# Kernel optimization log

Measured on AMD Instinct MI355X. Metric: run time of the kernel, lower is better.

The kernel has to match this reference:

```python
import jax, jax.numpy as jnp
import numpy as np

N = 50000      # num nodes
E = 400000     # num directed edges
IN = 128       # in_channels
H = 256        # hidden_channels
OUT = 128      # out_channels
LN_EPS = 1e-5


def setup_inputs() -> dict:
    key = jax.random.key(0)
    ks = jax.random.split(key, 12)
    x = jax.random.normal(ks[0], (N, IN), jnp.float32)
    edge_index = jax.random.randint(ks[1], (2, E), 0, N, jnp.int32)

    def lin(k, fi, fo):
        return jax.random.normal(k, (fi, fo), jnp.float32) / jnp.sqrt(jnp.float32(fi))

    return {
        "x": x,
        "edge_index": edge_index,
        "W1": lin(ks[2], IN, H),  "b1": jnp.zeros((H,), jnp.float32),
        "W2": lin(ks[3], H, H),   "b2": jnp.zeros((H,), jnp.float32),
        "W3": lin(ks[4], H, H),   "b3": jnp.zeros((H,), jnp.float32),
        "W4": lin(ks[5], H, OUT), "b4": jnp.zeros((OUT,), jnp.float32),
        "g1": jnp.ones((H,), jnp.float32),   "be1": jnp.zeros((H,), jnp.float32),
        "g2": jnp.ones((H,), jnp.float32),   "be2": jnp.zeros((H,), jnp.float32),
        "g3": jnp.ones((H,), jnp.float32),   "be3": jnp.zeros((H,), jnp.float32),
        "g4": jnp.ones((OUT,), jnp.float32), "be4": jnp.zeros((OUT,), jnp.float32),
    }


def layer_norm(h, g, b):
    m = jnp.mean(h, axis=-1, keepdims=True)
    v = jnp.mean(jnp.square(h - m), axis=-1, keepdims=True)
    return (h - m) * jax.lax.rsqrt(v + LN_EPS) * g + b


def gcn_conv(h, W, b, src, dst, dinv):
    # PyG GCNConv: add self-loops, norm = deg^-1/2[src] * deg^-1/2[dst]
    h = h @ W                                             # [N, F_out]
    norm = (dinv[src] * dinv[dst])[:, None]               # [E, 1]
    msg = h[src] * norm                                   # [E, F_out] irregular gather
    agg = jax.ops.segment_sum(msg, dst, num_segments=N)   # scatter-add
    agg = agg + h * jnp.square(dinv)[:, None]             # self-loop term
    return agg + b


def reference(x, edge_index, W1, b1, W2, b2, W3, b3, W4, b4,
              g1, be1, g2, be2, g3, be3, g4, be4):
    src, dst = edge_index[0], edge_index[1]
    # degree (incl. self-loop) from destination index, as in PyG gcn_norm
    deg = jax.ops.segment_sum(jnp.ones((E,), jnp.float32), dst, num_segments=N) + 1.0
    dinv = jax.lax.rsqrt(deg)

    h = gcn_conv(x, W1, b1, src, dst, dinv)
    h = jax.nn.relu(layer_norm(h, g1, be1))   # dropout = identity (eval)
    h = gcn_conv(h, W2, b2, src, dst, dinv)
    h = jax.nn.relu(layer_norm(h, g2, be2))
    h = gcn_conv(h, W3, b3, src, dst, dinv)
    h = jax.nn.relu(layer_norm(h, g3, be3))
    h = gcn_conv(h, W4, b4, src, dst, dinv)
    h = layer_norm(h, g4, be4)
    return h
```

## Files before the change

kernel.cpp:

```cpp
#include <hip/hip_runtime.h>

#define NN 50000
#define NEDGE 400000
#define MPAD 50048
#define NB 196
constexpr float LN_EPS = 1e-5f;

typedef __attribute__((ext_vector_type(8))) short bf16x8;
typedef __attribute__((ext_vector_type(4))) float f32x4;
typedef __attribute__((ext_vector_type(8))) unsigned short ushort8v;

__device__ __forceinline__ unsigned short f2bf(float f) {
  unsigned int u = __float_as_uint(f);
  u += 0x7FFFu + ((u >> 16) & 1u);
  return (unsigned short)(u >> 16);
}
__device__ __forceinline__ float bf2f(unsigned short u) {
  return __uint_as_float(((unsigned int)u) << 16);
}

__global__ __launch_bounds__(256) void k_prep(
    const float* __restrict__ W1, const float* __restrict__ W2,
    const float* __restrict__ W3, const float* __restrict__ W4,
    unsigned short* __restrict__ Wt1, unsigned short* __restrict__ Wt2,
    unsigned short* __restrict__ Wt3, unsigned short* __restrict__ Wt4,
    const float* __restrict__ x, unsigned short* __restrict__ xB,
    int* __restrict__ cnt) {
  const int b = blockIdx.x;
  const int n = threadIdx.x;
  if (b < 128) {
    Wt1[(size_t)n * 128 + b] = f2bf(W1[(size_t)b * 256 + n]);
  } else if (b < 384) {
    const int k = b - 128;
    Wt2[(size_t)n * 256 + k] = f2bf(W2[(size_t)k * 256 + n]);
  } else if (b < 640) {
    const int k = b - 384;
    Wt3[(size_t)n * 256 + k] = f2bf(W3[(size_t)k * 256 + n]);
  } else if (b < 896) {
    const int k = b - 640;
    if (n < 128) Wt4[(size_t)n * 256 + k] = f2bf(W4[(size_t)k * 128 + n]);
  } else if (b < 7146) {
    const int i = (b - 896) * 256 + n;
    float4 v = reinterpret_cast<const float4*>(x)[i];
    ushort4 o; o.x = f2bf(v.x); o.y = f2bf(v.y); o.z = f2bf(v.z); o.w = f2bf(v.w);
    reinterpret_cast<ushort4*>(xB)[i] = o;
  } else {
    const int i = (b - 7146) * 256 + n;
    if (i < NN) cnt[i] = 0;
  }
}

__global__ void k_count(const int* __restrict__ dst, int* __restrict__ cnt) {
  int e = blockIdx.x * blockDim.x + threadIdx.x;
  if (e < NEDGE) atomicAdd(&cnt[dst[e]], 1);
}

__global__ __launch_bounds__(256) void k_bsum(const int* __restrict__ cnt,
                                              int* __restrict__ bsum,
                                              float* __restrict__ dinv) {
  const int i = blockIdx.x * 256 + threadIdx.x;
  int v = 0;
  if (i < NN) {
    v = cnt[i];
    dinv[i] = rsqrtf((float)v + 1.0f);
  }
  int s = v;
#pragma unroll
  for (int off = 32; off > 0; off >>= 1) s += __shfl_xor(s, off);
  __shared__ int wsum[4];
  if ((threadIdx.x & 63) == 0) wsum[threadIdx.x >> 6] = s;
  __syncthreads();
  if (threadIdx.x == 0) bsum[blockIdx.x] = wsum[0] + wsum[1] + wsum[2] + wsum[3];
}

__global__ __launch_bounds__(256) void k_bapply(const int* __restrict__ cnt,
                                                const int* __restrict__ bsum,
                                                int* __restrict__ rowptr,
                                                int* __restrict__ cursor) {
  __shared__ int sOff[NB];
  __shared__ int wsum[4], woff[4];
  const int t = threadIdx.x;
  const int lane = t & 63, wid = t >> 6;

  {
    int v = (t < NB) ? bsum[t] : 0;
    int inc = v;
    for (int off = 1; off < 64; off <<= 1) {
      int y = __shfl_up(inc, off);
      if (lane >= off) inc += y;
    }
    if (lane == 63) wsum[wid] = inc;
    __syncthreads();
    if (t == 0) {
      int run = 0;
      for (int w = 0; w < 4; ++w) { woff[w] = run; run += wsum[w]; }
    }
    __syncthreads();
    if (t < NB) sOff[t] = woff[wid] + inc - v;
  }
  __syncthreads();

  const int i = blockIdx.x * 256 + t;
  int v = (i < NN) ? cnt[i] : 0;
  int inc = v;
  for (int off = 1; off < 64; off <<= 1) {
    int y = __shfl_up(inc, off);
    if (lane >= off) inc += y;
  }
  if (lane == 63) wsum[wid] = inc;
  __syncthreads();
  if (t == 0) {
    int run = 0;
    for (int w = 0; w < 4; ++w) { woff[w] = run; run += wsum[w]; }
  }
  __syncthreads();
  if (i < NN) {
    const int rp = sOff[blockIdx.x] + woff[wid] + inc - v;
    rowptr[i] = rp;
    cursor[i] = rp;
  }
  if (blockIdx.x == 0 && t == 0) rowptr[NN] = NEDGE;
}

__global__ void k_fill(const int* __restrict__ src, const int* __restrict__ dst,
                       const float* __restrict__ dinv, int* __restrict__ cursor,
                       int2* __restrict__ eidx2) {
  int e = blockIdx.x * blockDim.x + threadIdx.x;
  if (e >= NEDGE) return;
  const int d = dst[e];
  const int s = src[e];
  const int p = atomicAdd(&cursor[d], 1);
  eidx2[p] = make_int2(s, __float_as_int(dinv[s] * dinv[d]));
}

template<int F, int NPW, int MODE>
__global__ __launch_bounds__(256) void k_gather(
    const int* __restrict__ rowptr, const int2* __restrict__ eidx2,
    const float* __restrict__ dinv, const unsigned short* __restrict__ h,
    void* __restrict__ outv, const float* __restrict__ bias,
    const float* __restrict__ gamma, const float* __restrict__ beta) {
  constexpr int LPN = 64 / NPW;
  static_assert(F / LPN == 8, "16B per lane");
  const int tid = threadIdx.x;
  const int lane = tid & 63;
  const int sub = lane / LPN;
  const int slane = lane % LPN;
  const int n = blockIdx.x * (4 * NPW) + (tid >> 6) * NPW + sub;
  const bool valid = n < NN;

  int e = 0, end = 0;
  float dn = 0.f;
  if (valid) {
    dn = dinv[n];
    e = rowptr[n];
    end = rowptr[n + 1];
  }

  float acc[8];
  ushort8v r[8];
#pragma unroll
  for (int u = 0; u < 8; ++u) r[u] = (ushort8v)0;
  {
    ushort8v r0 = (ushort8v)0;
    if (valid) r0 = *reinterpret_cast<const ushort8v*>(h + (size_t)n * F + slane * 8);
    const float sw = dn * dn;
#pragma unroll
    for (int j = 0; j < 8; ++j) acc[j] = bf2f(r0[j]) * sw;
  }

  while (__ballot(e < end)) {
    float wgt[8];
#pragma unroll
    for (int u = 0; u < 8; ++u) {
      wgt[u] = 0.f;
      if (e + u < end) {
        const int2 p = eidx2[e + u];
        wgt[u] = __int_as_float(p.y);
        r[u] = *reinterpret_cast<const ushort8v*>(h + (size_t)p.x * F + slane * 8);
      }
    }
#pragma unroll
    for (int u = 0; u < 8; ++u)
#pragma unroll
      for (int j = 0; j < 8; ++j)
        acc[j] += wgt[u] * bf2f(r[u][j]);
    e += 8;
  }

  if (!valid) return;

  if constexpr (MODE == 0) {
    ushort8v o;
#pragma unroll
    for (int j = 0; j < 8; ++j) o[j] = f2bf(acc[j]);
    *reinterpret_cast<ushort8v*>((unsigned short*)outv + (size_t)n * F + slane * 8) = o;
  } else {
    const float4 b0 = *reinterpret_cast<const float4*>(bias + slane * 8);
    const float4 b1 = *reinterpret_cast<const float4*>(bias + slane * 8 + 4);
    acc[0] += b0.x; acc[1] += b0.y; acc[2] += b0.z; acc[3] += b0.w;
    acc[4] += b1.x; acc[5] += b1.y; acc[6] += b1.z; acc[7] += b1.w;
    float s = 0.f, q = 0.f;
#pragma unroll
    for (int j = 0; j < 8; ++j) { s += acc[j]; q = fmaf(acc[j], acc[j], q); }
#pragma unroll
    for (int off = 1; off < 16; off <<= 1) {
      s += __shfl_xor(s, off);
      q += __shfl_xor(q, off);
    }
    const float mean = s * (1.0f / 128.0f);
    const float var = q * (1.0f / 128.0f) - mean * mean;
    const float inv = rsqrtf(var + LN_EPS);
    const float4 g0 = *reinterpret_cast<const float4*>(gamma + slane * 8);
    const float4 g1 = *reinterpret_cast<const float4*>(gamma + slane * 8 + 4);
    const float4 e0 = *reinterpret_cast<const float4*>(beta + slane * 8);
    const float4 e1 = *reinterpret_cast<const float4*>(beta + slane * 8 + 4);
    float4 o0, o1;
    o0.x = (acc[0] - mean) * inv * g0.x + e0.x;
    o0.y = (acc[1] - mean) * inv * g0.y + e0.y;
    o0.z = (acc[2] - mean) * inv * g0.z + e0.z;
    o0.w = (acc[3] - mean) * inv * g0.w + e0.w;
    o1.x = (acc[4] - mean) * inv * g1.x + e1.x;
    o1.y = (acc[5] - mean) * inv * g1.y + e1.y;
    o1.z = (acc[6] - mean) * inv * g1.z + e1.z;
    o1.w = (acc[7] - mean) * inv * g1.w + e1.w;
    float* out = (float*)outv + (size_t)n * 128 + slane * 8;
    *reinterpret_cast<float4*>(out) = o0;
    *reinterpret_cast<float4*>(out + 4) = o1;
  }
}

template<int K, int N, bool LNFUSE>
__global__ __launch_bounds__(256) void k_mgemm(const unsigned short* __restrict__ A,
                                               const unsigned short* __restrict__ Bt,
                                               const float* __restrict__ bias,
                                               const float* __restrict__ gamma,
                                               const float* __restrict__ beta,
                                               unsigned short* __restrict__ out) {
  constexpr int NT = N / 64;
  constexpr int KS = K / 32;
  __shared__ __align__(16) unsigned short As[64 * K];

  const int tid = threadIdx.x;
  const int lane = tid & 63;
  const int w = tid >> 6;
  const int m0 = blockIdx.x * 64;

#pragma unroll
  for (int i = 0; i < KS; ++i) {
    const int o = (i * 256 + tid) * 16;
    const int row = o / (2 * K);
    const int inb = o % (2 * K);
    uint4 val = *reinterpret_cast<const uint4*>(
        (const char*)A + (size_t)(m0 + row) * (2 * K) + inb);
    const int dsto = o ^ ((row & 7) << 4);
    *reinterpret_cast<uint4*>((char*)As + dsto) = val;
  }
  __syncthreads();

  f32x4 acc[4][NT];
#pragma unroll
  for (int mt = 0; mt < 4; ++mt)
#pragma unroll
    for (int nt = 0; nt < NT; ++nt) acc[mt][nt] = (f32x4){0.f, 0.f, 0.f, 0.f};

  const int nw0 = w * (N / 4);
  const int arow = lane & 15;
  const int kgrp = (lane >> 4) * 8;

  for (int ks = 0; ks < KS; ++ks) {
    bf16x8 af[4];
#pragma unroll
    for (int mt = 0; mt < 4; ++mt) {
      const int r = mt * 16 + arow;
      int boff = (r * K + ks * 32 + kgrp) * 2;
      boff ^= (r & 7) << 4;
      af[mt] = *reinterpret_cast<const bf16x8*>((const char*)As + boff);
    }
    bf16x8 bfr[NT];
#pragma unroll
    for (int nt = 0; nt < NT; ++nt) {
      const int n = nw0 + nt * 16 + arow;
      bfr[nt] = *reinterpret_cast<const bf16x8*>(Bt + (size_t)n * K + ks * 32 + kgrp);
    }
#pragma unroll
    for (int mt = 0; mt < 4; ++mt)
#pragma unroll
      for (int nt = 0; nt < NT; ++nt)
        acc[mt][nt] = __builtin_amdgcn_mfma_f32_16x16x32_bf16(af[mt], bfr[nt], acc[mt][nt], 0, 0, 0);
  }

  const int g = lane >> 4;
  const int cl = lane & 15;

  if constexpr (LNFUSE) {
    float gv[NT], bev[NT];
#pragma unroll
    for (int nt = 0; nt < NT; ++nt) {
      const int c = nw0 + nt * 16 + cl;
      const float bv = bias[c];
      gv[nt] = gamma[c];
      bev[nt] = beta[c];
#pragma unroll
      for (int mt = 0; mt < 4; ++mt)
#pragma unroll
        for (int reg = 0; reg < 4; ++reg) acc[mt][nt][reg] += bv;
    }
    __shared__ float sS[4][64];
    __shared__ float sQ[4][64];
    float ps[4][4], pq[4][4];
#pragma unroll
    for (int mt = 0; mt < 4; ++mt) {
#pragma unroll
      for (int reg = 0; reg < 4; ++reg) {
        float s = 0.f, q = 0.f;
#pragma unroll
        for (int nt = 0; nt < NT; ++nt) {
          const float v = acc[mt][nt][reg];
          s += v; q = fmaf(v, v, q);
        }
#pragma unroll
        for (int off = 1; off < 16; off <<= 1) {
          s += __shfl_xor(s, off);
          q += __shfl_xor(q, off);
        }
        ps[mt][reg] = s; pq[mt][reg] = q;
      }
    }
    if (cl == 0) {
#pragma unroll
      for (int mt = 0; mt < 4; ++mt)
#pragma unroll
        for (int reg = 0; reg < 4; ++reg) {
          sS[w][mt * 16 + g * 4 + reg] = ps[mt][reg];
          sQ[w][mt * 16 + g * 4 + reg] = pq[mt][reg];
        }
    }
    __syncthreads();
#pragma unroll
    for (int mt = 0; mt < 4; ++mt) {
#pragma unroll
      for (int reg = 0; reg < 4; ++reg) {
        const int rr = mt * 16 + g * 4 + reg;
        const int r = m0 + rr;
        const float S = sS[0][rr] + sS[1][rr] + sS[2][rr] + sS[3][rr];
        const float Q = sQ[0][rr] + sQ[1][rr] + sQ[2][rr] + sQ[3][rr];
        const float mean = S * (1.0f / N);
        const float var = Q * (1.0f / N) - mean * mean;
        const float inv = rsqrtf(var + LN_EPS);
        if (r < NN) {
#pragma unroll
          for (int nt = 0; nt < NT; ++nt) {
            const int c = nw0 + nt * 16 + cl;
            const float o = fmaxf((acc[mt][nt][reg] - mean) * inv * gv[nt] + bev[nt], 0.f);
            out[(size_t)r * N + c] = f2bf(o);
          }
        }
      }
    }
  } else {
#pragma unroll
    for (int mt = 0; mt < 4; ++mt) {
#pragma unroll
      for (int nt = 0; nt < NT; ++nt) {
        const int c = nw0 + nt * 16 + cl;
#pragma unroll
        for (int reg = 0; reg < 4; ++reg) {
          const int r = m0 + mt * 16 + g * 4 + reg;
          if (r < NN) out[(size_t)r * N + c] = f2bf(acc[mt][nt][reg]);
        }
      }
    }
  }
}

extern "C" void kernel_launch(void* const* d_in, const int* in_sizes, int n_in,
                              void* d_out, int out_size, void* d_ws, size_t ws_size,
                              hipStream_t stream) {
  const float* x   = (const float*)d_in[0];
  const int*   ei  = (const int*)d_in[1];
  const float* W1  = (const float*)d_in[2];
  const float* b1  = (const float*)d_in[3];
  const float* W2  = (const float*)d_in[4];
  const float* b2  = (const float*)d_in[5];
  const float* W3  = (const float*)d_in[6];
  const float* b3  = (const float*)d_in[7];
  const float* W4  = (const float*)d_in[8];
  const float* b4  = (const float*)d_in[9];
  const float* g1  = (const float*)d_in[10];
  const float* be1 = (const float*)d_in[11];
  const float* g2  = (const float*)d_in[12];
  const float* be2 = (const float*)d_in[13];
  const float* g3  = (const float*)d_in[14];
  const float* be3 = (const float*)d_in[15];
  const float* g4  = (const float*)d_in[16];
  const float* be4 = (const float*)d_in[17];

  const int* src = ei;
  const int* dst = ei + NEDGE;

  char* ws = (char*)d_ws;
  int*   cnt    = (int*)(ws + 0);
  int*   cursor = (int*)(ws + 204800);
  int*   rowptr = (int*)(ws + 409600);
  float* dinv   = (float*)(ws + 614400);
  int*   bsum   = (int*)(ws + 819200);
  int2*  eidx2  = (int2*)(ws + 827392);
  unsigned short* Wt1 = (unsigned short*)(ws + 4030464);
  unsigned short* Wt2 = (unsigned short*)(ws + 4096000);
  unsigned short* Wt3 = (unsigned short*)(ws + 4227072);
  unsigned short* Wt4 = (unsigned short*)(ws + 4358144);
  unsigned short* xB  = (unsigned short*)(ws + 4423680);
  unsigned short* aggB = (unsigned short*)(ws + 17235968);
  unsigned short* hB   = (unsigned short*)(ws + 42860544);
  unsigned short* t4B  = (unsigned short*)(ws + 68485120);
  float* out = (float*)d_out;

  const int MB = (NN + 63) / 64;

  k_prep<<<7342, 256, 0, stream>>>(W1, W2, W3, W4, Wt1, Wt2, Wt3, Wt4, x, xB, cnt);
  k_count<<<(NEDGE + 255) / 256, 256, 0, stream>>>(dst, cnt);
  k_bsum<<<NB, 256, 0, stream>>>(cnt, bsum, dinv);
  k_bapply<<<NB, 256, 0, stream>>>(cnt, bsum, rowptr, cursor);
  k_fill<<<(NEDGE + 255) / 256, 256, 0, stream>>>(src, dst, dinv, cursor, eidx2);

  k_gather<128, 4, 0><<<(NN + 15) / 16, 256, 0, stream>>>(rowptr, eidx2, dinv, xB, aggB, nullptr, nullptr, nullptr);
  k_mgemm<128, 256, true><<<MB, 256, 0, stream>>>(aggB, Wt1, b1, g1, be1, hB);

  k_gather<256, 2, 0><<<(NN + 7) / 8, 256, 0, stream>>>(rowptr, eidx2, dinv, hB, aggB, nullptr, nullptr, nullptr);
  k_mgemm<256, 256, true><<<MB, 256, 0, stream>>>(aggB, Wt2, b2, g2, be2, hB);

  k_gather<256, 2, 0><<<(NN + 7) / 8, 256, 0, stream>>>(rowptr, eidx2, dinv, hB, aggB, nullptr, nullptr, nullptr);
  k_mgemm<256, 256, true><<<MB, 256, 0, stream>>>(aggB, Wt3, b3, g3, be3, hB);

  k_mgemm<256, 128, false><<<MB, 256, 0, stream>>>(hB, Wt4, nullptr, nullptr, nullptr, t4B);
  k_gather<128, 4, 1><<<(NN + 15) / 16, 256, 0, stream>>>(rowptr, eidx2, dinv, t4B, out, b4, g4, be4);
}
```

Baseline: 287.7 us.

## Sort nodes by in-degree so gather wavefronts process similar-degree nodes

Builds a degree histogram (capped at 63), scans it, and creates a node permutation that groups nodes with equal in-degree. The gather kernels then process nodes in that order, so nodes sharing a wavefront have similar edge counts and divergence from uneven loop lengths drops. In exchange there is an extra small kernel, more atomics during CSR setup, and scattered output row writes and self-row reads, since neighbouring lanes now touch non-adjacent nodes.

```diff
diff --git a/kernel.cpp b/kernel.cpp
--- a/kernel.cpp
+++ b/kernel.cpp
@@ -25,7 +25,7 @@
     unsigned short* __restrict__ Wt1, unsigned short* __restrict__ Wt2,
     unsigned short* __restrict__ Wt3, unsigned short* __restrict__ Wt4,
     const float* __restrict__ x, unsigned short* __restrict__ xB,
-    int* __restrict__ cnt) {
+    int* __restrict__ cnt, int* __restrict__ dhist) {
   const int b = blockIdx.x;
   const int n = threadIdx.x;
   if (b < 128) {
@@ -47,6 +47,7 @@
   } else {
     const int i = (b - 7146) * 256 + n;
     if (i < NN) cnt[i] = 0;
+    if (b == 7146 && n < 64) dhist[n] = 0;
   }
 }
 
@@ -57,12 +58,14 @@
 
 __global__ __launch_bounds__(256) void k_bsum(const int* __restrict__ cnt,
                                               int* __restrict__ bsum,
-                                              float* __restrict__ dinv) {
+                                              float* __restrict__ dinv,
+                                              int* __restrict__ dhist) {
   const int i = blockIdx.x * 256 + threadIdx.x;
   int v = 0;
   if (i < NN) {
     v = cnt[i];
     dinv[i] = rsqrtf((float)v + 1.0f);
+    atomicAdd(&dhist[v < 63 ? v : 63], 1);
   }
   int s = v;
 #pragma unroll
@@ -73,10 +76,26 @@
   if (threadIdx.x == 0) bsum[blockIdx.x] = wsum[0] + wsum[1] + wsum[2] + wsum[3];
 }
 
+__global__ void k_dscan(const int* __restrict__ dhist, int* __restrict__ dbase,
+                        int* __restrict__ dcur) {
+  const int t = threadIdx.x;
+  const int v = dhist[t];
+  int inc = v;
+  for (int off = 1; off < 64; off <<= 1) {
+    int y = __shfl_up(inc, off);
+    if (t >= off) inc += y;
+  }
+  dbase[t] = inc - v;
+  dcur[t] = inc - v;
+}
+
 __global__ __launch_bounds__(256) void k_bapply(const int* __restrict__ cnt,
                                                 const int* __restrict__ bsum,
                                                 int* __restrict__ rowptr,
-                                                int* __restrict__ cursor) {
+                                                int* __restrict__ cursor,
+                                                const int* __restrict__ dbase,
+                                                int* __restrict__ dcur,
+                                                int* __restrict__ perm) {
   __shared__ int sOff[NB];
   __shared__ int wsum[4], woff[4];
   const int t = threadIdx.x;
@@ -118,6 +137,9 @@
     const int rp = sOff[blockIdx.x] + woff[wid] + inc - v;
     rowptr[i] = rp;
     cursor[i] = rp;
+    const int bin = v < 63 ? v : 63;
+    const int pos = atomicAdd(&dcur[bin], 1);
+    perm[pos] = i;
   }
   if (blockIdx.x == 0 && t == 0) rowptr[NN] = NEDGE;
 }
@@ -135,6 +157,7 @@
 
 template<int F, int NPW, int MODE>
 __global__ __launch_bounds__(256) void k_gather(
+    const int* __restrict__ perm,
     const int* __restrict__ rowptr, const int2* __restrict__ eidx2,
     const float* __restrict__ dinv, const unsigned short* __restrict__ h,
     void* __restrict__ outv, const float* __restrict__ bias,
@@ -145,8 +168,9 @@
   const int lane = tid & 63;
   const int sub = lane / LPN;
   const int slane = lane % LPN;
-  const int n = blockIdx.x * (4 * NPW) + (tid >> 6) * NPW + sub;
-  const bool valid = n < NN;
+  const int gidx = blockIdx.x * (4 * NPW) + (tid >> 6) * NPW + sub;
+  const bool valid = gidx < NN;
+  const int n = valid ? perm[gidx] : 0;
 
   int e = 0, end = 0;
   float dn = 0.f;
@@ -404,34 +428,39 @@
   int*   rowptr = (int*)(ws + 409600);
   float* dinv   = (float*)(ws + 614400);
   int*   bsum   = (int*)(ws + 819200);
-  int2*  eidx2  = (int2*)(ws + 827392);
-  unsigned short* Wt1 = (unsigned short*)(ws + 4030464);
-  unsigned short* Wt2 = (unsigned short*)(ws + 4096000);
-  unsigned short* Wt3 = (unsigned short*)(ws + 4227072);
-  unsigned short* Wt4 = (unsigned short*)(ws + 4358144);
-  unsigned short* xB  = (unsigned short*)(ws + 4423680);
-  unsigned short* aggB = (unsigned short*)(ws + 17235968);
-  unsigned short* hB   = (unsigned short*)(ws + 42860544);
-  unsigned short* t4B  = (unsigned short*)(ws + 68485120);
+  int*   dhist  = (int*)(ws + 823296);
+  int*   dbase  = (int*)(ws + 823552);
+  int*   dcur   = (int*)(ws + 823808);
+  int*   perm   = (int*)(ws + 824320);
+  int2*  eidx2  = (int2*)(ws + 1048576);
+  unsigned short* Wt1 = (unsigned short*)(ws + 4300800);
+  unsigned short* Wt2 = (unsigned short*)(ws + 4366336);
+  unsigned short* Wt3 = (unsigned short*)(ws + 4497408);
+  unsigned short* Wt4 = (unsigned short*)(ws + 4628480);
+  unsigned short* xB  = (unsigned short*)(ws + 4694016);
+  unsigned short* aggB = (unsigned short*)(ws + 17506304);
+  unsigned short* hB   = (unsigned short*)(ws + 43130880);
+  unsigned short* t4B  = (unsigned short*)(ws + 68755456);
   float* out = (float*)d_out;
 
   const int MB = (NN + 63) / 64;
 
-  k_prep<<<7342, 256, 0, stream>>>(W1, W2, W3, W4, Wt1, Wt2, Wt3, Wt4, x, xB, cnt);
+  k_prep<<<7342, 256, 0, stream>>>(W1, W2, W3, W4, Wt1, Wt2, Wt3, Wt4, x, xB, cnt, dhist);
   k_count<<<(NEDGE + 255) / 256, 256, 0, stream>>>(dst, cnt);
-  k_bsum<<<NB, 256, 0, stream>>>(cnt, bsum, dinv);
-  k_bapply<<<NB, 256, 0, stream>>>(cnt, bsum, rowptr, cursor);
+  k_bsum<<<NB, 256, 0, stream>>>(cnt, bsum, dinv, dhist);
+  k_dscan<<<1, 64, 0, stream>>>(dhist, dbase, dcur);
+  k_bapply<<<NB, 256, 0, stream>>>(cnt, bsum, rowptr, cursor, dbase, dcur, perm);
   k_fill<<<(NEDGE + 255) / 256, 256, 0, stream>>>(src, dst, dinv, cursor, eidx2);
 
-  k_gather<128, 4, 0><<<(NN + 15) / 16, 256, 0, stream>>>(rowptr, eidx2, dinv, xB, aggB, nullptr, nullptr, nullptr);
+  k_gather<128, 4, 0><<<(NN + 15) / 16, 256, 0, stream>>>(perm, rowptr, eidx2, dinv, xB, aggB, nullptr, nullptr, nullptr);
   k_mgemm<128, 256, true><<<MB, 256, 0, stream>>>(aggB, Wt1, b1, g1, be1, hB);
 
-  k_gather<256, 2, 0><<<(NN + 7) / 8, 256, 0, stream>>>(rowptr, eidx2, dinv, hB, aggB, nullptr, nullptr, nullptr);
+  k_gather<256, 2, 0><<<(NN + 7) / 8, 256, 0, stream>>>(perm, rowptr, eidx2, dinv, hB, aggB, nullptr, nullptr, nullptr);
   k_mgemm<256, 256, true><<<MB, 256, 0, stream>>>(aggB, Wt2, b2, g2, be2, hB);
 
-  k_gather<256, 2, 0><<<(NN + 7) / 8, 256, 0, stream>>>(rowptr, eidx2, dinv, hB, aggB, nullptr, nullptr, nullptr);
+  k_gather<256, 2, 0><<<(NN + 7) / 8, 256, 0, stream>>>(perm, rowptr, eidx2, dinv, hB, aggB, nullptr, nullptr, nullptr);
   k_mgemm<256, 256, true><<<MB, 256, 0, stream>>>(aggB, Wt3, b3, g3, be3, hB);
 
   k_mgemm<256, 128, false><<<MB, 256, 0, stream>>>(hB, Wt4, nullptr, nullptr, nullptr, t4B);
-  k_gather<128, 4, 1><<<(NN + 15) / 16, 256, 0, stream>>>(rowptr, eidx2, dinv, t4B, out, b4, g4, be4);
-}
+  k_gather<128, 4, 1><<<(NN + 15) / 16, 256, 0, stream>>>(perm, rowptr, eidx2, dinv, t4B, out, b4, g4, be4);
+}
```

Measured after the change: 630.7 us (median of 2 runs). +119.2%, slower.
